# Kernel tuning notes

Hardware: AMD Instinct MI355X
Metric: run time of the kernel (lower is better)

The kernel has to match this reference:

```python
import jax, jax.numpy as jnp
import numpy as np

EPS = 1e-06


def setup_inputs() -> dict:
    key = jax.random.key(0)
    k1, k2 = jax.random.split(key)
    B, T, E = 4, 4096, 1024
    M = E // 2
    x = jax.random.normal(k1, (B, T, E), dtype=jnp.float32)
    # causal mask: position i may attend to j <= i... note module multiplies K
    # (which is nonzero only for j >= i) by mask; a standard causal lower-tri
    # mask would zero everything but the diagonal. The module's bump kernel
    # looks FORWARD (diff = (j-i).clamp(min=0)), so the natural mask here is
    # upper-triangular (j >= i), i.e. the 'causal' mask for this pooling.
    mask = jnp.triu(jnp.ones((T, T), dtype=bool))
    gate_raw = jnp.full((M,), -3.0, dtype=jnp.float32)
    return {"x": x, "mask": mask, "gate_raw": gate_raw}


def reference(x, mask, gate_raw):
    B, T, E = x.shape
    dtype = x.dtype
    x_c = x[..., 0::2]                                  # (B, T, M) content channels

    # convex bump kernel K[i, j], nonzero for j >= i
    i = jnp.arange(T, dtype=dtype)[:, None]
    j = jnp.arange(T, dtype=dtype)[None, :]
    diff = jnp.maximum(j - i, 0.0)
    horizon = jnp.maximum(jnp.float32(T) - i, 1.0)
    u = jnp.minimum(diff / horizon, 1.0 - EPS)
    K = jnp.exp(1.0 - 1.0 / (1.0 - u * u + EPS))
    K = jnp.where(u >= 1.0 - EPS, jnp.asarray(EPS, dtype), K)

    K = K * mask.astype(dtype)
    K = K / jnp.maximum(K.sum(-1, keepdims=True), EPS)  # row-normalize

    phi = jnp.einsum('ij,bjm->bim', K, x_c)             # (B, T, M)
    gate = jax.nn.softplus(gate_raw)[None, None, :]     # (1, 1, M)
    out = x.at[..., 1::2].set(phi * gate)               # write phase channels
    return out
```

## Files before the change

kernel.cpp:

```cpp
#include <hip/hip_runtime.h>
#include <cstdint>
#include <cstddef>

#define Tdim 4096
#define Bdim 4
#define Edim 1024
#define Mdim 512
#define EPSF 1e-6f

typedef __bf16 bf16x8 __attribute__((ext_vector_type(8)));
typedef float f32x4 __attribute__((ext_vector_type(4)));

__device__ __forceinline__ unsigned short f2bf(float f) {
  union { float f; unsigned int u; } a; a.f = f;
  unsigned int r = a.u + 0x7fffu + ((a.u >> 16) & 1u);
  return (unsigned short)(r >> 16);
}

__device__ __forceinline__ float kernel_g(float dj, float inv_h) {
  float u = fminf(dj * inv_h, 1.0f - EPSF);
  return __expf(1.0f - 1.0f / (1.0f - u * u + EPSF));
}

typedef void __attribute__((address_space(1)))* gas1;
typedef void __attribute__((address_space(3)))* las3;
__device__ __forceinline__ void load_lds16(const void* g, void* l) {
  __builtin_amdgcn_global_load_lds((gas1)(g), (las3)(l), 16, 0, 0);
}


__global__ __launch_bounds__(256) void gate_kernel(const float* __restrict__ graw,
                                                   float* __restrict__ gate) {
  const int m = blockIdx.x * 256 + threadIdx.x;
  if (m < Mdim) {
    const float v = graw[m];
    gate[m] = fmaxf(v, 0.0f) + log1pf(__expf(-fabsf(v)));
  }
}

__global__ __launch_bounds__(256) void rowsum_kernel(float* __restrict__ inv_rowsum) {
  const int i = blockIdx.x;
  const int tid = threadIdx.x;
  const float inv_h = 1.0f / (float)(Tdim - i);
  float s = 0.0f;
  for (int j = i + tid; j < Tdim; j += 256)
    s += kernel_g((float)(j - i), inv_h);
#pragma unroll
  for (int off = 32; off; off >>= 1) s += __shfl_down(s, off);
  __shared__ float red[4];
  if ((tid & 63) == 0) red[tid >> 6] = s;
  __syncthreads();
  if (tid == 0) inv_rowsum[i] = 1.0f / (red[0] + red[1] + red[2] + red[3]);
}

__global__ __launch_bounds__(256) void kgen_kernel(const float* __restrict__ inv_rowsum,
                                                   unsigned short* __restrict__ Kmat) {
  const int i = blockIdx.y;
  const int j0 = (blockIdx.x * 256 + threadIdx.x) * 8;
  union { unsigned short u[8]; uint4 v; } pk;
  if (j0 + 7 < i) {
    pk.v = make_uint4(0u, 0u, 0u, 0u);
  } else {
    const float inv_h = 1.0f / (float)(Tdim - i);
    const float inv_s = inv_rowsum[i];
#pragma unroll
    for (int t = 0; t < 8; ++t) {
      const int j = j0 + t;
      float r = 0.0f;
      if (j >= i) r = kernel_g((float)(j - i), inv_h) * inv_s;
      pk.u[t] = f2bf(r);
    }
  }
  *reinterpret_cast<uint4*>(&Kmat[(size_t)i * Tdim + j0]) = pk.v;
}

__global__ __launch_bounds__(256) void extract_kernel(const float* __restrict__ x,
                                                      unsigned short* __restrict__ XcT) {
  __shared__ unsigned short Ls[32][68];
  const int j0 = blockIdx.x * 64;
  const int m0 = blockIdx.y * 32;
  const int b  = blockIdx.z;
  const int tid = threadIdx.x;
  const int q = tid & 15;
  const int jbase = tid >> 4;
#pragma unroll
  for (int it = 0; it < 4; ++it) {
    const int jj = jbase + it * 16;
    const size_t off = ((size_t)(b * Tdim + j0 + jj)) * Edim + 2 * m0 + 4 * q;
    const float4 v = *reinterpret_cast<const float4*>(&x[off]);
    Ls[2 * q][jj]     = f2bf(v.x);
    Ls[2 * q + 1][jj] = f2bf(v.z);
  }
  __syncthreads();
  const int ch = tid & 15;
  const int mb = tid >> 4;
#pragma unroll
  for (int it = 0; it < 2; ++it) {
    const int m = mb + it * 16;
    ushort4 uv;
    uv.x = Ls[m][4 * ch];
    uv.y = Ls[m][4 * ch + 1];
    uv.z = Ls[m][4 * ch + 2];
    uv.w = Ls[m][4 * ch + 3];
    *reinterpret_cast<ushort4*>(
        &XcT[((size_t)(b * Mdim + m0 + m)) * Tdim + j0 + 4 * ch]) = uv;
  }
}

__global__ __launch_bounds__(256) void gemm_kernel(
    const unsigned short* __restrict__ Kmat,
    const unsigned short* __restrict__ XcT,
    const float* __restrict__ x,
    const float* __restrict__ gate,
    float* __restrict__ out) {
  const int p  = blockIdx.x;
  const int i0 = p * 128;
  const int m0 = blockIdx.y * 128;
  const int b  = blockIdx.z;

  __shared__ unsigned short As[2][128 * 64];
  __shared__ unsigned short Bs[2][128 * 64];
  const int tid = threadIdx.x;
  const int w = tid >> 6;
  const int l = tid & 63;
  f32x4 acc[4][4] = {};
  const int wr = w >> 1, wc = w & 1;
  const unsigned short* Arow = Kmat + (size_t)i0 * Tdim;
  const unsigned short* Brow = XcT + ((size_t)b * Mdim + m0) * Tdim;
  const int srow  = l >> 3;
  const int sslot = l & 7;
  const int schunk = (sslot ^ srow) * 8;

#pragma unroll
  for (int t = 0; t < 4; ++t) {
    const int rr = (w * 4 + t) * 8 + srow;
    load_lds16(Arow + (size_t)rr * Tdim + (i0 + schunk), &As[0][(w * 4 + t) * 512]);
    load_lds16(Brow + (size_t)rr * Tdim + (i0 + schunk), &Bs[0][(w * 4 + t) * 512]);
  }

  int cur = 0;
  const int lr16 = l & 15;
  const int kq = l >> 4;
  for (int j0 = i0; j0 < Tdim; j0 += 64, cur ^= 1) {
    __syncthreads();
    const int jn = j0 + 64;
    if (jn < Tdim) {
#pragma unroll
      for (int t = 0; t < 4; ++t) {
        const int rr = (w * 4 + t) * 8 + srow;
        load_lds16(Arow + (size_t)rr * Tdim + (jn + schunk), &As[cur ^ 1][(w * 4 + t) * 512]);
        load_lds16(Brow + (size_t)rr * Tdim + (jn + schunk), &Bs[cur ^ 1][(w * 4 + t) * 512]);
      }
    }
#pragma unroll
    for (int kk = 0; kk < 2; ++kk) {
      bf16x8 af[4], bfr[4];
      const int chunk = kk * 4 + kq;
      const int slot = (chunk ^ (lr16 & 7)) * 8;
#pragma unroll
      for (int r = 0; r < 4; ++r)
        af[r] = *reinterpret_cast<const bf16x8*>(&As[cur][(wr * 64 + r * 16 + lr16) * 64 + slot]);
#pragma unroll
      for (int c = 0; c < 4; ++c)
        bfr[c] = *reinterpret_cast<const bf16x8*>(&Bs[cur][(wc * 64 + c * 16 + lr16) * 64 + slot]);
#pragma unroll
      for (int r = 0; r < 4; ++r)
#pragma unroll
        for (int c = 0; c < 4; ++c)
          acc[r][c] = __builtin_amdgcn_mfma_f32_16x16x32_bf16(af[r], bfr[c], acc[r][c], 0, 0, 0);
    }
  }

  const int lr = l & 15;
  const int lq = l >> 4;
#pragma unroll
  for (int r = 0; r < 4; ++r) {
    const int i = i0 + wr * 64 + r * 16 + lq * 4;
#pragma unroll
    for (int c = 0; c < 4; ++c) {
      const int m = m0 + wc * 64 + c * 16 + lr;
      const float gm = gate[m];
#pragma unroll
      for (int v = 0; v < 4; ++v) {
        const size_t o = ((size_t)(b * Tdim + i + v)) * Edim + 2 * m;
        const float2 xv = *reinterpret_cast<const float2*>(&x[o]);
        float2 res;
        res.x = xv.x;
        res.y = acc[r][c][v] * gm;
        *reinterpret_cast<float2*>(&out[o]) = res;
      }
    }
  }
}

__global__ __launch_bounds__(256) void fallback_kernel(const float* __restrict__ x,
                                                       const float* __restrict__ graw,
                                                       float* __restrict__ out) {
  const int i = blockIdx.x, b = blockIdx.y, tid = threadIdx.x;
  const float inv_h = 1.0f / (float)(Tdim - i);
  float s = 0.0f;
  for (int j = i + tid; j < Tdim; j += 256)
    s += kernel_g((float)(j - i), inv_h);
#pragma unroll
  for (int off = 32; off; off >>= 1) s += __shfl_down(s, off);
  __shared__ float red[4];
  __shared__ float sinv_sh;
  if ((tid & 63) == 0) red[tid >> 6] = s;
  __syncthreads();
  if (tid == 0) sinv_sh = 1.0f / (red[0] + red[1] + red[2] + red[3]);
  __syncthreads();
  const float sinv = sinv_sh;
  const float* xb = x + (size_t)b * Tdim * Edim;
  float a0 = 0.0f, a1 = 0.0f;
  const int m0 = tid, m1 = tid + 256;
  for (int j = i; j < Tdim; ++j) {
    const float wgt = kernel_g((float)(j - i), inv_h);
    const float* xr = xb + (size_t)j * Edim;
    a0 += wgt * xr[2 * m0];
    a1 += wgt * xr[2 * m1];
  }
  const float v0 = graw[m0], v1 = graw[m1];
  const float g0 = fmaxf(v0, 0.0f) + log1pf(__expf(-fabsf(v0)));
  const float g1 = fmaxf(v1, 0.0f) + log1pf(__expf(-fabsf(v1)));
  const size_t o = ((size_t)(b * Tdim + i)) * Edim;
  const float* xi = xb + (size_t)i * Edim;
  out[o + 2 * m0]     = xi[2 * m0];
  out[o + 2 * m0 + 1] = a0 * sinv * g0;
  out[o + 2 * m1]     = xi[2 * m1];
  out[o + 2 * m1 + 1] = a1 * sinv * g1;
}

extern "C" void kernel_launch(void* const* d_in, const int* in_sizes, int n_in,
                              void* d_out, int out_size, void* d_ws, size_t ws_size,
                              hipStream_t stream) {
  const float* x = (const float*)d_in[0];
  const float* gate_raw = (const float*)d_in[2];
  float* out = (float*)d_out;

  const size_t XcT_bytes = (size_t)Bdim * Mdim * Tdim * 2;
  const size_t K_bytes   = (size_t)Tdim * Tdim * 2;
  const size_t need = XcT_bytes + K_bytes + (size_t)(Tdim + Mdim) * sizeof(float);

  if (ws_size < need) {
    fallback_kernel<<<dim3(Tdim, Bdim), 256, 0, stream>>>(x, gate_raw, out);
    return;
  }

  char* ws = (char*)d_ws;
  unsigned short* XcT  = (unsigned short*)ws;
  unsigned short* Kmat = (unsigned short*)(ws + XcT_bytes);
  float* inv_rowsum    = (float*)(ws + XcT_bytes + K_bytes);
  float* gate          = inv_rowsum + Tdim;

  gate_kernel<<<dim3((Mdim + 255) / 256), 256, 0, stream>>>(gate_raw, gate);
  rowsum_kernel<<<dim3(Tdim), 256, 0, stream>>>(inv_rowsum);
  kgen_kernel<<<dim3(Tdim / (256 * 8), Tdim), 256, 0, stream>>>(inv_rowsum, Kmat);
  extract_kernel<<<dim3(Tdim / 64, Mdim / 32, Bdim), 256, 0, stream>>>(x, XcT);
  gemm_kernel<<<dim3(Tdim / 128, Mdim / 128, Bdim), 256, 0, stream>>>(Kmat, XcT, x, gate, out);
}
```

Measured before the change: 247.8 us.

## Generate bump-kernel tile on the fly inside GEMM instead of materializing K

Removes the separate kgen kernel and the 32 MB bf16 K matrix. Each GEMM block now computes its 128x64 K tile directly into LDS every iteration from the analytic formula and the per-row inverse sum, using a fast exp, a fast reciprocal and a packed bf16 conversion. The A operand is single-buffered with an extra barrier per iteration. Blocks are also remapped to a 1D grid that pairs long and short causal rows to balance load. This trades HBM traffic and one kernel launch for extra transcendental ALU work per tile and reduced overlap of the A path.

After: 290.2 us. 17.1% more time.

```diff
diff --git a/kernel.cpp b/kernel.cpp
--- a/kernel.cpp
+++ b/kernel.cpp
@@ -15,6 +15,11 @@
   union { float f; unsigned int u; } a; a.f = f;
   unsigned int r = a.u + 0x7fffu + ((a.u >> 16) & 1u);
   return (unsigned short)(r >> 16);
+}
+
+__device__ __forceinline__ unsigned int pack_bf16(float a, float b) {
+  union { float f; unsigned int u; } ua, ub; ua.f = a; ub.f = b;
+  return __builtin_amdgcn_perm(ub.u + 0x8000u, ua.u + 0x8000u, 0x07060302u);
 }
 
 __device__ __forceinline__ float kernel_g(float dj, float inv_h) {
@@ -51,27 +56,6 @@
   if ((tid & 63) == 0) red[tid >> 6] = s;
   __syncthreads();
   if (tid == 0) inv_rowsum[i] = 1.0f / (red[0] + red[1] + red[2] + red[3]);
-}
-
-__global__ __launch_bounds__(256) void kgen_kernel(const float* __restrict__ inv_rowsum,
-                                                   unsigned short* __restrict__ Kmat) {
-  const int i = blockIdx.y;
-  const int j0 = (blockIdx.x * 256 + threadIdx.x) * 8;
-  union { unsigned short u[8]; uint4 v; } pk;
-  if (j0 + 7 < i) {
-    pk.v = make_uint4(0u, 0u, 0u, 0u);
-  } else {
-    const float inv_h = 1.0f / (float)(Tdim - i);
-    const float inv_s = inv_rowsum[i];
-#pragma unroll
-    for (int t = 0; t < 8; ++t) {
-      const int j = j0 + t;
-      float r = 0.0f;
-      if (j >= i) r = kernel_g((float)(j - i), inv_h) * inv_s;
-      pk.u[t] = f2bf(r);
-    }
-  }
-  *reinterpret_cast<uint4*>(&Kmat[(size_t)i * Tdim + j0]) = pk.v;
 }
 
 __global__ __launch_bounds__(256) void extract_kernel(const float* __restrict__ x,
@@ -108,85 +92,121 @@
 }
 
 __global__ __launch_bounds__(256) void gemm_kernel(
-    const unsigned short* __restrict__ Kmat,
     const unsigned short* __restrict__ XcT,
+    const float* __restrict__ inv_rowsum,
     const float* __restrict__ x,
     const float* __restrict__ gate,
     float* __restrict__ out) {
-  const int p  = blockIdx.x;
+  const int id = blockIdx.x;
+  int p, mb;
+  if (id < 256) { p = id & 31; mb = id >> 5; }
+  else          { p = 31 - (id & 31); mb = 8 + ((id - 256) >> 5); }
   const int i0 = p * 128;
-  const int m0 = blockIdx.y * 128;
-  const int b  = blockIdx.z;
-
-  __shared__ unsigned short As[2][128 * 64];
+  const int m0 = (mb & 3) * 128;
+  const int b  = mb >> 2;
+
+  __shared__ unsigned short As[128 * 64];
   __shared__ unsigned short Bs[2][128 * 64];
   const int tid = threadIdx.x;
   const int w = tid >> 6;
   const int l = tid & 63;
   f32x4 acc[4][4] = {};
   const int wr = w >> 1, wc = w & 1;
-  const unsigned short* Arow = Kmat + (size_t)i0 * Tdim;
   const unsigned short* Brow = XcT + ((size_t)b * Mdim + m0) * Tdim;
   const int srow  = l >> 3;
   const int sslot = l & 7;
   const int schunk = (sslot ^ srow) * 8;
 
+  const int r = tid >> 1;
+  const int h = tid & 1;
+  const int i = i0 + r;
+  const float inv_h = __fdividef(1.0f, (float)(Tdim - i));
+  const float crow  = 2.7182818284590452f * inv_rowsum[i];
+  unsigned int* Aw = reinterpret_cast<unsigned int*>(As);
+
 #pragma unroll
   for (int t = 0; t < 4; ++t) {
     const int rr = (w * 4 + t) * 8 + srow;
-    load_lds16(Arow + (size_t)rr * Tdim + (i0 + schunk), &As[0][(w * 4 + t) * 512]);
     load_lds16(Brow + (size_t)rr * Tdim + (i0 + schunk), &Bs[0][(w * 4 + t) * 512]);
   }
 
-  int cur = 0;
   const int lr16 = l & 15;
   const int kq = l >> 4;
-  for (int j0 = i0; j0 < Tdim; j0 += 64, cur ^= 1) {
+  const int niter = (Tdim - i0) >> 6;
+  for (int jt = 0; jt < niter; ++jt) {
+    const int j0 = i0 + jt * 64;
+    const int cur = jt & 1;
     __syncthreads();
-    const int jn = j0 + 64;
-    if (jn < Tdim) {
+    if (jt + 1 < niter) {
+      const int jn = j0 + 64;
 #pragma unroll
       for (int t = 0; t < 4; ++t) {
         const int rr = (w * 4 + t) * 8 + srow;
-        load_lds16(Arow + (size_t)rr * Tdim + (jn + schunk), &As[cur ^ 1][(w * 4 + t) * 512]);
         load_lds16(Brow + (size_t)rr * Tdim + (jn + schunk), &Bs[cur ^ 1][(w * 4 + t) * 512]);
       }
     }
+    {
+      const int dj0 = j0 + h * 32 - i;
+      const float u0 = (float)dj0 * inv_h;
+      const bool diag = (jt < 2);
+#pragma unroll
+      for (int cc = 0; cc < 4; ++cc) {
+        float v[8];
+#pragma unroll
+        for (int k = 0; k < 8; ++k) {
+          const int e = cc * 8 + k;
+          const float u = fmaf((float)e, inv_h, u0);
+          const float d = fmaf(-u, u, 1.000001f);
+          const float rr = __fdividef(1.0f, d);
+          float val = crow * __expf(-rr);
+          if (diag && (dj0 + e) < 0) val = 0.0f;
+          v[k] = val;
+        }
+        uint4 pk;
+        pk.x = pack_bf16(v[0], v[1]);
+        pk.y = pack_bf16(v[2], v[3]);
+        pk.z = pack_bf16(v[4], v[5]);
+        pk.w = pack_bf16(v[6], v[7]);
+        const int slot = ((h * 4 + cc) ^ (r & 7));
+        *reinterpret_cast<uint4*>(&Aw[r * 32 + slot * 4]) = pk;
+      }
+    }
+    __syncthreads();
 #pragma unroll
     for (int kk = 0; kk < 2; ++kk) {
       bf16x8 af[4], bfr[4];
       const int chunk = kk * 4 + kq;
       const int slot = (chunk ^ (lr16 & 7)) * 8;
 #pragma unroll
-      for (int r = 0; r < 4; ++r)
-        af[r] = *reinterpret_cast<const bf16x8*>(&As[cur][(wr * 64 + r * 16 + lr16) * 64 + slot]);
+      for (int rr2 = 0; rr2 < 4; ++rr2)
+        af[rr2] = *reinterpret_cast<const bf16x8*>(&As[(wr * 64 + rr2 * 16 + lr16) * 64 + slot]);
 #pragma unroll
       for (int c = 0; c < 4; ++c)
         bfr[c] = *reinterpret_cast<const bf16x8*>(&Bs[cur][(wc * 64 + c * 16 + lr16) * 64 + slot]);
 #pragma unroll
-      for (int r = 0; r < 4; ++r)
+      for (int rr2 = 0; rr2 < 4; ++rr2)
 #pragma unroll
         for (int c = 0; c < 4; ++c)
-          acc[r][c] = __builtin_amdgcn_mfma_f32_16x16x32_bf16(af[r], bfr[c], acc[r][c], 0, 0, 0);
+          acc[rr2][c] = __builtin_amdgcn_mfma_f32_16x16x32_bf16(af[rr2], bfr[c], acc[rr2][c], 0, 0, 0);
     }
   }
 
   const int lr = l & 15;
   const int lq = l >> 4;
 #pragma unroll
-  for (int r = 0; r < 4; ++r) {
-    const int i = i0 + wr * 64 + r * 16 + lq * 4;
+  for (int rr2 = 0; rr2 < 4; ++rr2) {
+    const int ii = i0 + wr * 64 + rr2 * 16 + lq * 4;
 #pragma unroll
     for (int c = 0; c < 4; ++c) {
       const int m = m0 + wc * 64 + c * 16 + lr;
       const float gm = gate[m];
 #pragma unroll
       for (int v = 0; v < 4; ++v) {
-        const size_t o = ((size_t)(b * Tdim + i + v)) * Edim + 2 * m;
+        const size_t o = ((size_t)(b * Tdim + ii + v)) * Edim + 2 * m;
         const float2 xv = *reinterpret_cast<const float2*>(&x[o]);
         float2 res;
         res.x = xv.x;
-        res.y = acc[r][c][v] * gm;
+        res.y = acc[rr2][c][v] * gm;
         *reinterpret_cast<float2*>(&out[o]) = res;
       }
     }
@@ -238,8 +258,7 @@
   float* out = (float*)d_out;
 
   const size_t XcT_bytes = (size_t)Bdim * Mdim * Tdim * 2;
-  const size_t K_bytes   = (size_t)Tdim * Tdim * 2;
-  const size_t need = XcT_bytes + K_bytes + (size_t)(Tdim + Mdim) * sizeof(float);
+  const size_t need = XcT_bytes + (size_t)(Tdim + Mdim) * sizeof(float);
 
   if (ws_size < need) {
     fallback_kernel<<<dim3(Tdim, Bdim), 256, 0, stream>>>(x, gate_raw, out);
@@ -248,13 +267,11 @@
 
   char* ws = (char*)d_ws;
   unsigned short* XcT  = (unsigned short*)ws;
-  unsigned short* Kmat = (unsigned short*)(ws + XcT_bytes);
-  float* inv_rowsum    = (float*)(ws + XcT_bytes + K_bytes);
+  float* inv_rowsum    = (float*)(ws + XcT_bytes);
   float* gate          = inv_rowsum + Tdim;
 
   gate_kernel<<<dim3((Mdim + 255) / 256), 256, 0, stream>>>(gate_raw, gate);
   rowsum_kernel<<<dim3(Tdim), 256, 0, stream>>>(inv_rowsum);
-  kgen_kernel<<<dim3(Tdim / (256 * 8), Tdim), 256, 0, stream>>>(inv_rowsum, Kmat);
   extract_kernel<<<dim3(Tdim / 64, Mdim / 32, Bdim), 256, 0, stream>>>(x, XcT);
-  gemm_kernel<<<dim3(Tdim / 128, Mdim / 128, Bdim), 256, 0, stream>>>(Kmat, XcT, x, gate, out);
-}
+  gemm_kernel<<<dim3(512), 256, 0, stream>>>(XcT, inv_rowsum, x, gate, out);
+}
```

## Fuse K generation, rowsum, extraction into one prep kernel and reorder GEMM blocks

Applied to the files above, without the earlier changes.

Merges the rowsum, K-matrix generation and x-content extraction kernels into a single prep launch. Each row's bump values are cached in shared memory so the exponential is computed once instead of twice. The softplus gate is computed inline in the GEMM epilogue, removing the gate kernel and its workspace. The GEMM grid is flattened and remapped to pair light and heavy row tiles of the triangular K, which is meant to cut launch overhead and balance load. The rowsum epsilon clamp and a cheaper bf16 pack with different rounding slightly change numerics.

Result: faster. 227.9 us (-8.0%).

```diff
diff --git a/kernel.cpp b/kernel.cpp
--- a/kernel.cpp
+++ b/kernel.cpp
@@ -17,6 +17,11 @@
   return (unsigned short)(r >> 16);
 }
 
+__device__ __forceinline__ unsigned int pack_bf16(float a, float b) {
+  union { float f; unsigned int u; } ua, ub; ua.f = a; ub.f = b;
+  return __builtin_amdgcn_perm(ub.u + 0x8000u, ua.u + 0x8000u, 0x07060302u);
+}
+
 __device__ __forceinline__ float kernel_g(float dj, float inv_h) {
   float u = fminf(dj * inv_h, 1.0f - EPSF);
   return __expf(1.0f - 1.0f / (1.0f - u * u + EPSF));
@@ -28,82 +33,74 @@
   __builtin_amdgcn_global_load_lds((gas1)(g), (las3)(l), 16, 0, 0);
 }
 
-
-__global__ __launch_bounds__(256) void gate_kernel(const float* __restrict__ graw,
-                                                   float* __restrict__ gate) {
-  const int m = blockIdx.x * 256 + threadIdx.x;
-  if (m < Mdim) {
-    const float v = graw[m];
-    gate[m] = fmaxf(v, 0.0f) + log1pf(__expf(-fabsf(v)));
-  }
-}
-
-__global__ __launch_bounds__(256) void rowsum_kernel(float* __restrict__ inv_rowsum) {
-  const int i = blockIdx.x;
+__global__ __launch_bounds__(256) void prep_kernel(const float* __restrict__ x,
+                                                   unsigned short* __restrict__ Kmat,
+                                                   unsigned short* __restrict__ XcT) {
+  __shared__ float smem[4104];
   const int tid = threadIdx.x;
-  const float inv_h = 1.0f / (float)(Tdim - i);
-  float s = 0.0f;
-  for (int j = i + tid; j < Tdim; j += 256)
-    s += kernel_g((float)(j - i), inv_h);
-#pragma unroll
-  for (int off = 32; off; off >>= 1) s += __shfl_down(s, off);
-  __shared__ float red[4];
-  if ((tid & 63) == 0) red[tid >> 6] = s;
-  __syncthreads();
-  if (tid == 0) inv_rowsum[i] = 1.0f / (red[0] + red[1] + red[2] + red[3]);
-}
-
-__global__ __launch_bounds__(256) void kgen_kernel(const float* __restrict__ inv_rowsum,
-                                                   unsigned short* __restrict__ Kmat) {
-  const int i = blockIdx.y;
-  const int j0 = (blockIdx.x * 256 + threadIdx.x) * 8;
-  union { unsigned short u[8]; uint4 v; } pk;
-  if (j0 + 7 < i) {
-    pk.v = make_uint4(0u, 0u, 0u, 0u);
+  const int id = blockIdx.x;
+  if (id < Tdim) {
+    const int i = id;
+    const float inv_h = __fdividef(1.0f, (float)(Tdim - i));
+    float s = 0.0f;
+    for (int j = i + tid; j < Tdim; j += 256) {
+      const float g = kernel_g((float)(j - i), inv_h);
+      smem[j] = g;
+      s += g;
+    }
+#pragma unroll
+    for (int off = 32; off; off >>= 1) s += __shfl_down(s, off);
+    if ((tid & 63) == 0) smem[4096 + (tid >> 6)] = s;
+    __syncthreads();
+    const float inv_s = __fdividef(
+        1.0f, fmaxf(smem[4096] + smem[4097] + smem[4098] + smem[4099], EPSF));
+    unsigned short* row = Kmat + (size_t)i * Tdim;
+#pragma unroll
+    for (int q = tid; q < 512; q += 256) {
+      const int j8 = q * 8;
+      float v[8];
+#pragma unroll
+      for (int k = 0; k < 8; ++k) {
+        const int j = j8 + k;
+        v[k] = (j >= i) ? smem[j] * inv_s : 0.0f;
+      }
+      uint4 pk;
+      pk.x = pack_bf16(v[0], v[1]);
+      pk.y = pack_bf16(v[2], v[3]);
+      pk.z = pack_bf16(v[4], v[5]);
+      pk.w = pack_bf16(v[6], v[7]);
+      *reinterpret_cast<uint4*>(&row[j8]) = pk;
+    }
   } else {
-    const float inv_h = 1.0f / (float)(Tdim - i);
-    const float inv_s = inv_rowsum[i];
-#pragma unroll
-    for (int t = 0; t < 8; ++t) {
-      const int j = j0 + t;
-      float r = 0.0f;
-      if (j >= i) r = kernel_g((float)(j - i), inv_h) * inv_s;
-      pk.u[t] = f2bf(r);
-    }
-  }
-  *reinterpret_cast<uint4*>(&Kmat[(size_t)i * Tdim + j0]) = pk.v;
-}
-
-__global__ __launch_bounds__(256) void extract_kernel(const float* __restrict__ x,
-                                                      unsigned short* __restrict__ XcT) {
-  __shared__ unsigned short Ls[32][68];
-  const int j0 = blockIdx.x * 64;
-  const int m0 = blockIdx.y * 32;
-  const int b  = blockIdx.z;
-  const int tid = threadIdx.x;
-  const int q = tid & 15;
-  const int jbase = tid >> 4;
-#pragma unroll
-  for (int it = 0; it < 4; ++it) {
-    const int jj = jbase + it * 16;
-    const size_t off = ((size_t)(b * Tdim + j0 + jj)) * Edim + 2 * m0 + 4 * q;
-    const float4 v = *reinterpret_cast<const float4*>(&x[off]);
-    Ls[2 * q][jj]     = f2bf(v.x);
-    Ls[2 * q + 1][jj] = f2bf(v.z);
-  }
-  __syncthreads();
-  const int ch = tid & 15;
-  const int mb = tid >> 4;
-#pragma unroll
-  for (int it = 0; it < 2; ++it) {
-    const int m = mb + it * 16;
-    ushort4 uv;
-    uv.x = Ls[m][4 * ch];
-    uv.y = Ls[m][4 * ch + 1];
-    uv.z = Ls[m][4 * ch + 2];
-    uv.w = Ls[m][4 * ch + 3];
-    *reinterpret_cast<ushort4*>(
-        &XcT[((size_t)(b * Mdim + m0 + m)) * Tdim + j0 + 4 * ch]) = uv;
+    const int eid = id - Tdim;
+    const int j0 = (eid & 63) * 64;
+    const int m0 = ((eid >> 6) & 15) * 32;
+    const int b  = eid >> 10;
+    unsigned short* Ls = reinterpret_cast<unsigned short*>(smem);
+    const int q = tid & 15;
+    const int jbase = tid >> 4;
+#pragma unroll
+    for (int it = 0; it < 4; ++it) {
+      const int jj = jbase + it * 16;
+      const size_t off = ((size_t)(b * Tdim + j0 + jj)) * Edim + 2 * m0 + 4 * q;
+      const float4 v = *reinterpret_cast<const float4*>(&x[off]);
+      Ls[(2 * q) * 68 + jj]     = f2bf(v.x);
+      Ls[(2 * q + 1) * 68 + jj] = f2bf(v.z);
+    }
+    __syncthreads();
+    const int ch = tid & 15;
+    const int mb = tid >> 4;
+#pragma unroll
+    for (int it = 0; it < 2; ++it) {
+      const int m = mb + it * 16;
+      ushort4 uv;
+      uv.x = Ls[m * 68 + 4 * ch];
+      uv.y = Ls[m * 68 + 4 * ch + 1];
+      uv.z = Ls[m * 68 + 4 * ch + 2];
+      uv.w = Ls[m * 68 + 4 * ch + 3];
+      *reinterpret_cast<ushort4*>(
+          &XcT[((size_t)(b * Mdim + m0 + m)) * Tdim + j0 + 4 * ch]) = uv;
+    }
   }
 }
 
@@ -111,12 +108,16 @@
     const unsigned short* __restrict__ Kmat,
     const unsigned short* __restrict__ XcT,
     const float* __restrict__ x,
-    const float* __restrict__ gate,
+    const float* __restrict__ graw,
     float* __restrict__ out) {
-  const int p  = blockIdx.x;
+  const int id = blockIdx.x;
+  int p;
+  if (id < 256) p = id >> 4;
+  else          p = 31 - ((id - 256) >> 4);
+  const int mb = id & 15;
   const int i0 = p * 128;
-  const int m0 = blockIdx.y * 128;
-  const int b  = blockIdx.z;
+  const int m0 = (mb & 3) * 128;
+  const int b  = mb >> 2;
 
   __shared__ unsigned short As[2][128 * 64];
   __shared__ unsigned short Bs[2][128 * 64];
@@ -173,20 +174,25 @@
 
   const int lr = l & 15;
   const int lq = l >> 4;
+  float gm[4];
+#pragma unroll
+  for (int c = 0; c < 4; ++c) {
+    const float v = graw[m0 + wc * 64 + c * 16 + lr];
+    gm[c] = fmaxf(v, 0.0f) + __logf(1.0f + __expf(-fabsf(v)));
+  }
 #pragma unroll
   for (int r = 0; r < 4; ++r) {
-    const int i = i0 + wr * 64 + r * 16 + lq * 4;
+    const int ii = i0 + wr * 64 + r * 16 + lq * 4;
 #pragma unroll
     for (int c = 0; c < 4; ++c) {
       const int m = m0 + wc * 64 + c * 16 + lr;
-      const float gm = gate[m];
 #pragma unroll
       for (int v = 0; v < 4; ++v) {
-        const size_t o = ((size_t)(b * Tdim + i + v)) * Edim + 2 * m;
+        const size_t o = ((size_t)(b * Tdim + ii + v)) * Edim + 2 * m;
         const float2 xv = *reinterpret_cast<const float2*>(&x[o]);
         float2 res;
         res.x = xv.x;
-        res.y = acc[r][c][v] * gm;
+        res.y = acc[r][c][v] * gm[c];
         *reinterpret_cast<float2*>(&out[o]) = res;
       }
     }
@@ -239,7 +245,7 @@
 
   const size_t XcT_bytes = (size_t)Bdim * Mdim * Tdim * 2;
   const size_t K_bytes   = (size_t)Tdim * Tdim * 2;
-  const size_t need = XcT_bytes + K_bytes + (size_t)(Tdim + Mdim) * sizeof(float);
+  const size_t need = XcT_bytes + K_bytes;
 
   if (ws_size < need) {
     fallback_kernel<<<dim3(Tdim, Bdim), 256, 0, stream>>>(x, gate_raw, out);
@@ -249,12 +255,7 @@
   char* ws = (char*)d_ws;
   unsigned short* XcT  = (unsigned short*)ws;
   unsigned short* Kmat = (unsigned short*)(ws + XcT_bytes);
-  float* inv_rowsum    = (float*)(ws + XcT_bytes + K_bytes);
-  float* gate          = inv_rowsum + Tdim;
-
-  gate_kernel<<<dim3((Mdim + 255) / 256), 256, 0, stream>>>(gate_raw, gate);
-  rowsum_kernel<<<dim3(Tdim), 256, 0, stream>>>(inv_rowsum);
-  kgen_kernel<<<dim3(Tdim / (256 * 8), Tdim), 256, 0, stream>>>(inv_rowsum, Kmat);
-  extract_kernel<<<dim3(Tdim / 64, Mdim / 32, Bdim), 256, 0, stream>>>(x, XcT);
-  gemm_kernel<<<dim3(Tdim / 128, Mdim / 128, Bdim), 256, 0, stream>>>(Kmat, XcT, x, gate, out);
-}
+
+  prep_kernel<<<dim3(2 * Tdim), 256, 0, stream>>>(x, Kmat, XcT);
+  gemm_kernel<<<dim3(512), 256, 0, stream>>>(Kmat, XcT, x, gate_raw, out);
+}
```
